# Kernel tuning notes

Hardware: AMD Instinct MI355X
Metric: run time of the kernel (lower is better)

The kernel has to match this reference:

```python
import jax, jax.numpy as jnp
import numpy as np

N_NODES = 100000
N_EDGES = 1600000
D = 128
N_LAYERS = 3
BN_EPS = 1e-5
NORM_EPS = 1e-12


def setup_inputs() -> dict:
    key = jax.random.key(0)
    ks = jax.random.split(key, 4)
    x = jax.random.normal(ks[0], (N_NODES, D), dtype=jnp.float32)
    edge_index = jax.random.randint(ks[1], (2, N_EDGES), 0, N_NODES, dtype=jnp.int32)
    W1 = jax.random.normal(ks[2], (N_LAYERS, D, D), dtype=jnp.float32) * (1.0 / np.sqrt(D))
    W2 = jax.random.normal(ks[3], (N_LAYERS, D, D), dtype=jnp.float32) * (1.0 / np.sqrt(D))
    return {
        "x": x,
        "edge_index": edge_index,
        "W1": W1,
        "b1": jnp.zeros((N_LAYERS, D), jnp.float32),
        "g1": jnp.ones((N_LAYERS, D), jnp.float32),
        "be1": jnp.zeros((N_LAYERS, D), jnp.float32),
        "W2": W2,
        "b2": jnp.zeros((N_LAYERS, D), jnp.float32),
        "g_out": jnp.ones((N_LAYERS - 1, D), jnp.float32),
        "b_out": jnp.zeros((N_LAYERS - 1, D), jnp.float32),
    }


def _batchnorm(h, gamma, beta):
    # BatchNorm1d in training mode: biased batch statistics over nodes.
    mu = jnp.mean(h, axis=0)
    var = jnp.var(h, axis=0)
    return (h - mu) * jax.lax.rsqrt(var + BN_EPS) * gamma + beta


def reference(x, edge_index, W1, b1, g1, be1, W2, b2, g_out, b_out):
    src, dst = edge_index[0], edge_index[1]
    h = x
    for i in range(N_LAYERS):
        # GINConv, eps=0: (1+eps)*x + sum of neighbor messages (scatter-add)
        agg = jax.ops.segment_sum(h[src], dst, num_segments=N_NODES)
        h = h + agg
        # inner MLP: Linear -> BN -> ReLU -> Linear
        h = h @ W1[i] + b1[i]
        h = jax.nn.relu(_batchnorm(h, g1[i], be1[i]))
        h = h @ W2[i] + b2[i]
        if i < N_LAYERS - 1:
            h = jax.nn.relu(_batchnorm(h, g_out[i], b_out[i]))
    # F.normalize(p=2, dim=-1) clamps the norm at 1e-12
    norm = jnp.linalg.norm(h, axis=-1, keepdims=True)
    return h / jnp.maximum(norm, NORM_EPS)
```

## Files before the change

### kernel.cpp

```cpp
#include <hip/hip_runtime.h>

#define M_NODES 100000
#define PADM 100032
#define DIM 128
#define N_EDGES_TOT 1600000
#define NBKT 256
#define NPB 391
#define BKT_CAP 8192
#define INVN 1e-5f
#define NREP 8

typedef unsigned int uint;
typedef unsigned short ushort;
typedef __attribute__((ext_vector_type(8))) short bf16x8;
typedef __attribute__((ext_vector_type(4))) float f32x4;

__device__ __forceinline__ float bflo(uint u) { return __uint_as_float(u << 16); }
__device__ __forceinline__ float bfhi(uint u) { return __uint_as_float(u & 0xffff0000u); }
__device__ __forceinline__ float bf2f(ushort h) { return __uint_as_float(((uint)h) << 16); }
__device__ __forceinline__ ushort f2bf(float f) {
    uint u = __float_as_uint(f);
    return (ushort)((u + 0x7fffu + ((u >> 16) & 1u)) >> 16);
}

__global__ void k_zerof(float* p, int n) {
    int i = blockIdx.x * 256 + threadIdx.x;
    if (i < n) p[i] = 0.f;
}

__global__ void k_cvt(const float* __restrict__ x, ushort* __restrict__ xb,
                      int n4) {
    int i = blockIdx.x * 256 + threadIdx.x;
    if (i >= n4) return;
    float4 v = ((const float4*)x)[i];
    uint2 r;
    r.x = (uint)f2bf(v.x) | ((uint)f2bf(v.y) << 16);
    r.y = (uint)f2bf(v.z) | ((uint)f2bf(v.w) << 16);
    ((uint2*)xb)[i] = r;
}

__global__ void k_wprep(const float* __restrict__ W1,
                        const float* __restrict__ W2, ushort* __restrict__ Wh,
                        ushort* __restrict__ Wl) {
    int i = blockIdx.x * 256 + threadIdx.x;
    if (i >= 6 * 16384) return;
    int l = i >> 14;
    int r = i & 16383;
    int n = r >> 7, k = r & 127;
    const float* W = (l < 3) ? (W1 + l * 16384) : (W2 + (l - 3) * 16384);
    float w = W[k * 128 + n];
    ushort h = f2bf(w);
    Wh[i] = h;
    Wl[i] = f2bf(w - bf2f(h));
}

__global__ void k_bhist(const int* __restrict__ dst, int* __restrict__ cntM,
                        int nE, int nChunks) {
    __shared__ int h[NBKT];
    const int chunk = blockIdx.x, t = threadIdx.x;
    h[t] = 0;
    __syncthreads();
    const int e0 = chunk * 2048;
#pragma unroll
    for (int k = 0; k < 8; ++k) {
        int e = e0 + k * 256 + t;
        if (e < nE) atomicAdd(&h[dst[e] / NPB], 1);
    }
    __syncthreads();
    cntM[t * nChunks + chunk] = h[t];
}

__global__ void k_scanA(int* __restrict__ cnt, int* __restrict__ bsum, int n) {
    __shared__ int s[256];
    int t = threadIdx.x, i = blockIdx.x * 256 + t;
    int v = (i < n) ? cnt[i] : 0;
    s[t] = v;
    __syncthreads();
#pragma unroll
    for (int o = 1; o < 256; o <<= 1) {
        int a = (t >= o) ? s[t - o] : 0;
        __syncthreads();
        s[t] += a;
        __syncthreads();
    }
    if (i < n) cnt[i] = s[t] - v;
    if (t == 255) bsum[blockIdx.x] = s[255];
}

__global__ void k_scanB(int* bsum, int nB) {
    __shared__ int s[1024];
    int t = threadIdx.x;
    int v = (t < nB) ? bsum[t] : 0;
    s[t] = v;
    __syncthreads();
#pragma unroll
    for (int o = 1; o < 1024; o <<= 1) {
        int a = (t >= o) ? s[t - o] : 0;
        __syncthreads();
        s[t] += a;
        __syncthreads();
    }
    if (t < nB) bsum[t] = s[t] - v;
}

__global__ void k_scanC(int* __restrict__ excl, const int* __restrict__ bsum) {
    int i = blockIdx.x * 256 + threadIdx.x;
    excl[i] += bsum[blockIdx.x];
}

__global__ void k_pairs(const int* __restrict__ src, const int* __restrict__ dst,
                        const int* __restrict__ exclM, int2* __restrict__ pairs,
                        int nE, int nChunks) {
    __shared__ int base[NBKT];
    const int chunk = blockIdx.x, t = threadIdx.x;
    base[t] = exclM[t * nChunks + chunk];
    __syncthreads();
    const int e0 = chunk * 2048;
#pragma unroll
    for (int k = 0; k < 8; ++k) {
        int e = e0 + k * 256 + t;
        if (e < nE) {
            int d = dst[e];
            int pos = atomicAdd(&base[d / NPB], 1);
            pairs[pos] = make_int2(d, src[e]);
        }
    }
}

__global__ void k_csrD(const int2* __restrict__ pairs,
                       const int* __restrict__ exclM, int nChunks,
                       int* __restrict__ rowptr, int* __restrict__ srcs,
                       int nE) {
    __shared__ int cnt[512];
    __shared__ int scn[512];
    __shared__ int sl[BKT_CAP];
    const int b = blockIdx.x, t = threadIdx.x;
    const int base = exclM[b * nChunks];
    const int next = (b == NBKT - 1) ? nE : exclM[(b + 1) * nChunks];
    const int count = next - base;
    const int nodeBase = b * NPB;
    const int nNodes = min(NPB, M_NODES - nodeBase);
    cnt[t] = 0;
    cnt[t + 256] = 0;
    __syncthreads();
    for (int i = t; i < count; i += 256)
        atomicAdd(&cnt[pairs[base + i].x - nodeBase], 1);
    __syncthreads();
    scn[t] = cnt[t];
    scn[t + 256] = cnt[t + 256];
    __syncthreads();
#pragma unroll
    for (int o = 1; o < 512; o <<= 1) {
        int a0 = (t >= o) ? scn[t - o] : 0;
        int a1 = scn[t + 256 - o];
        __syncthreads();
        scn[t] += a0;
        scn[t + 256] += a1;
        __syncthreads();
    }
    int o0 = scn[t] - cnt[t];
    int o1 = scn[t + 256] - cnt[t + 256];
    __syncthreads();
    cnt[t] = o0;
    cnt[t + 256] = o1;
    if (t < nNodes) rowptr[nodeBase + t] = base + o0;
    if (t + 256 < nNodes) rowptr[nodeBase + t + 256] = base + o1;
    if (b == 0 && t == 0) rowptr[M_NODES] = nE;
    __syncthreads();
    const bool inLds = (count <= BKT_CAP);
    for (int i = t; i < count; i += 256) {
        int2 p = pairs[base + i];
        int pos = atomicAdd(&cnt[p.x - nodeBase], 1);
        if (inLds) sl[pos] = p.y;
        else srcs[base + pos] = p.y;
    }
    __syncthreads();
    if (inLds)
        for (int i = t; i < count; i += 256) srcs[base + i] = sl[i];
}

__global__ void k_gather(const ushort* __restrict__ h,
                         const int* __restrict__ rowptr,
                         const int* __restrict__ srcs,
                         const float* __restrict__ bnstats,
                         const float* __restrict__ gamma,
                         const float* __restrict__ beta,
                         ushort* __restrict__ AGh, ushort* __restrict__ AGl,
                         int M) {
    int t = threadIdx.x;
    int node = blockIdx.x * 16 + (t >> 4);
    if (node >= M) return;
    int c = (t & 15) * 8;
    const bool bn = (bnstats != nullptr);
    float sc[8], sh[8];
    if (bn) {
#pragma unroll
        for (int e = 0; e < 8; ++e) { sc[e] = 0.f; sh[e] = 0.f; }
        for (int r = 0; r < NREP; ++r) {
            const float* bp = bnstats + r * 256;
#pragma unroll
            for (int e = 0; e < 8; ++e) {
                sc[e] += bp[c + e];
                sh[e] += bp[128 + c + e];
            }
        }
#pragma unroll
        for (int e = 0; e < 8; ++e) {
            float mu = sc[e] * INVN;
            float var = sh[e] * INVN - mu * mu;
            float s = gamma[c + e] * rsqrtf(var + 1e-5f);
            sc[e] = s;
            sh[e] = beta[c + e] - mu * s;
        }
    }
    int beg = rowptr[node];
    int end = rowptr[node + 1];

    float a[8], b[8];
    {
        uint4 v = *(const uint4*)(h + (size_t)node * DIM + c);
        uint u[4] = {v.x, v.y, v.z, v.w};
#pragma unroll
        for (int e = 0; e < 4; ++e) {
            a[2 * e] = bflo(u[e]);
            a[2 * e + 1] = bfhi(u[e]);
        }
        if (bn) {
#pragma unroll
            for (int e = 0; e < 8; ++e)
                a[e] = fmaxf(fmaf(a[e], sc[e], sh[e]), 0.f);
        }
#pragma unroll
        for (int e = 0; e < 8; ++e) b[e] = 0.f;
    }

    int j = beg;
    for (; j + 4 <= end; j += 4) {
        int s0 = srcs[j], s1 = srcs[j + 1], s2 = srcs[j + 2], s3 = srcs[j + 3];
        uint4 g0 = *(const uint4*)(h + (size_t)s0 * DIM + c);
        uint4 g1 = *(const uint4*)(h + (size_t)s1 * DIM + c);
        uint4 g2 = *(const uint4*)(h + (size_t)s2 * DIM + c);
        uint4 g3 = *(const uint4*)(h + (size_t)s3 * DIM + c);
        uint u0[4] = {g0.x, g0.y, g0.z, g0.w};
        uint u1[4] = {g1.x, g1.y, g1.z, g1.w};
        uint u2[4] = {g2.x, g2.y, g2.z, g2.w};
        uint u3[4] = {g3.x, g3.y, g3.z, g3.w};
        if (bn) {
#pragma unroll
            for (int e = 0; e < 4; ++e) {
                a[2 * e] += fmaxf(fmaf(bflo(u0[e]), sc[2 * e], sh[2 * e]), 0.f);
                a[2 * e + 1] += fmaxf(fmaf(bfhi(u0[e]), sc[2 * e + 1], sh[2 * e + 1]), 0.f);
                b[2 * e] += fmaxf(fmaf(bflo(u1[e]), sc[2 * e], sh[2 * e]), 0.f);
                b[2 * e + 1] += fmaxf(fmaf(bfhi(u1[e]), sc[2 * e + 1], sh[2 * e + 1]), 0.f);
                a[2 * e] += fmaxf(fmaf(bflo(u2[e]), sc[2 * e], sh[2 * e]), 0.f);
                a[2 * e + 1] += fmaxf(fmaf(bfhi(u2[e]), sc[2 * e + 1], sh[2 * e + 1]), 0.f);
                b[2 * e] += fmaxf(fmaf(bflo(u3[e]), sc[2 * e], sh[2 * e]), 0.f);
                b[2 * e + 1] += fmaxf(fmaf(bfhi(u3[e]), sc[2 * e + 1], sh[2 * e + 1]), 0.f);
            }
        } else {
#pragma unroll
            for (int e = 0; e < 4; ++e) {
                a[2 * e] += bflo(u0[e]) + bflo(u2[e]);
                a[2 * e + 1] += bfhi(u0[e]) + bfhi(u2[e]);
                b[2 * e] += bflo(u1[e]) + bflo(u3[e]);
                b[2 * e + 1] += bfhi(u1[e]) + bfhi(u3[e]);
            }
        }
    }
    for (; j < end; ++j) {
        int s = srcs[j];
        uint4 g = *(const uint4*)(h + (size_t)s * DIM + c);
        uint u[4] = {g.x, g.y, g.z, g.w};
        if (bn) {
#pragma unroll
            for (int e = 0; e < 4; ++e) {
                a[2 * e] += fmaxf(fmaf(bflo(u[e]), sc[2 * e], sh[2 * e]), 0.f);
                a[2 * e + 1] += fmaxf(fmaf(bfhi(u[e]), sc[2 * e + 1], sh[2 * e + 1]), 0.f);
            }
        } else {
#pragma unroll
            for (int e = 0; e < 4; ++e) {
                a[2 * e] += bflo(u[e]);
                a[2 * e + 1] += bfhi(u[e]);
            }
        }
    }
    uint ho[4], lo4[4];
#pragma unroll
    for (int e = 0; e < 4; ++e) {
        float v0 = a[2 * e] + b[2 * e];
        float v1 = a[2 * e + 1] + b[2 * e + 1];
        ushort h0 = f2bf(v0), h1 = f2bf(v1);
        ho[e] = (uint)h0 | ((uint)h1 << 16);
        lo4[e] = (uint)f2bf(v0 - bf2f(h0)) | ((uint)f2bf(v1 - bf2f(h1)) << 16);
    }
    size_t ix = (size_t)node * DIM + c;
    *(uint4*)(AGh + ix) = make_uint4(ho[0], ho[1], ho[2], ho[3]);
    *(uint4*)(AGl + ix) = make_uint4(lo4[0], lo4[1], lo4[2], lo4[3]);
}

__global__ void __launch_bounds__(256, 3) k_gemmA(
    ushort* __restrict__ Ah, const ushort* __restrict__ Al,
    const ushort* __restrict__ Wh, const ushort* __restrict__ Wl,
    const float* __restrict__ bias, float* __restrict__ statSlot, int M) {
    __shared__ ushort lds[16384];
    const int t = threadIdx.x;
    const int w = t >> 6, lane = t & 63, rq = lane >> 4, rc = lane & 15;
    const int row0 = blockIdx.x * 64;

    bf16x8 wh[4][2], wl[4][2];
#pragma unroll
    for (int kc = 0; kc < 4; ++kc)
#pragma unroll
        for (int jj = 0; jj < 2; ++jj) {
            size_t off = (size_t)(w * 32 + jj * 16 + rc) * DIM + kc * 32 + rq * 8;
            wh[kc][jj] = *(const bf16x8*)(Wh + off);
            wl[kc][jj] = *(const bf16x8*)(Wl + off);
        }

#pragma unroll
    for (int i = 0; i < 8; ++i) {
        int idx = t + i * 256;
        int pl = idx >> 10;
        int r = (idx >> 4) & 63;
        int cb = idx & 15;
        const ushort* p = pl ? Al : Ah;
        uint4 v = *(const uint4*)(p + (size_t)(row0 + r) * DIM + cb * 8);
        *(uint4*)((char*)lds + pl * 16384 + r * 256 +
                  ((cb * 16) ^ ((r & 15) << 4))) = v;
    }
    __syncthreads();

    f32x4 acc[4][2];
#pragma unroll
    for (int i = 0; i < 4; ++i)
#pragma unroll
        for (int jj = 0; jj < 2; ++jj) acc[i][jj] = (f32x4){0.f, 0.f, 0.f, 0.f};

#pragma unroll
    for (int kc = 0; kc < 4; ++kc) {
        const int kb = kc * 64 + rq * 16;
#pragma unroll
        for (int i = 0; i < 4; ++i) {
            int lr = i * 16 + rc;
            int so = lr * 256 + (kb ^ ((lr & 15) << 4));
            bf16x8 ah = *(const bf16x8*)((char*)lds + so);
            bf16x8 al = *(const bf16x8*)((char*)lds + 16384 + so);
#pragma unroll
            for (int jj = 0; jj < 2; ++jj) {
                acc[i][jj] = __builtin_amdgcn_mfma_f32_16x16x32_bf16(ah, wh[kc][jj], acc[i][jj], 0, 0, 0);
                acc[i][jj] = __builtin_amdgcn_mfma_f32_16x16x32_bf16(al, wh[kc][jj], acc[i][jj], 0, 0, 0);
                acc[i][jj] = __builtin_amdgcn_mfma_f32_16x16x32_bf16(ah, wl[kc][jj], acc[i][jj], 0, 0, 0);
            }
        }
    }

    float bc[2] = {bias[w * 32 + rc], bias[w * 32 + 16 + rc]};
    float csum[2] = {0.f, 0.f}, csq[2] = {0.f, 0.f};

    __syncthreads();
#pragma unroll
    for (int i = 0; i < 4; ++i)
#pragma unroll
        for (int r = 0; r < 4; ++r) {
            int lrow = i * 16 + rq * 4 + r;
            bool live = (row0 + lrow) < M;
#pragma unroll
            for (int jj = 0; jj < 2; ++jj) {
                float o = acc[i][jj][r] + bc[jj];
                int off = lrow * 256 +
                          (((w * 32 + jj * 16 + rc) * 2) ^ ((lrow & 15) << 4));
                *(ushort*)((char*)lds + off) = f2bf(o);
                if (live) { csum[jj] += o; csq[jj] += o * o; }
            }
        }
    __syncthreads();
    {
        int lrow = w * 16 + (lane & 15);
        int kq = lane >> 4;
        ushort* dH = Ah + (size_t)row0 * DIM;
#pragma unroll
        for (int kc = 0; kc < 4; ++kc) {
            int off = lrow * 256 + ((kc * 64 + kq * 16) ^ ((lrow & 15) << 4));
            uint4 H = *(uint4*)((char*)lds + off);
            size_t go = ((size_t)(w * 4 + kc) * 64 + lane) * 8;
            *(uint4*)(dH + go) = H;
        }
    }
#pragma unroll
    for (int jj = 0; jj < 2; ++jj) {
        csum[jj] += __shfl_xor(csum[jj], 16);
        csum[jj] += __shfl_xor(csum[jj], 32);
        csq[jj] += __shfl_xor(csq[jj], 16);
        csq[jj] += __shfl_xor(csq[jj], 32);
    }
    float* slot = statSlot + (blockIdx.x & (NREP - 1)) * 256;
    if (lane < 16) {
        atomicAdd(slot + w * 32 + rc, csum[0]);
        atomicAdd(slot + w * 32 + 16 + rc, csum[1]);
        atomicAdd(slot + 128 + w * 32 + rc, csq[0]);
        atomicAdd(slot + 128 + w * 32 + 16 + rc, csq[1]);
    }
}

__global__ void __launch_bounds__(256, 4) k_gemmB(
    const ushort* __restrict__ Ch,
    const ushort* __restrict__ Wh, const ushort* __restrict__ Wl,
    const float* __restrict__ bias, const float* __restrict__ bnstats,
    const float* __restrict__ gamma, const float* __restrict__ beta,
    ushort* __restrict__ Cb, float* __restrict__ outF,
    float* __restrict__ statSlot, int M) {
    __shared__ char smem[16384];
    const int t = threadIdx.x;
    const int w = t >> 6, lane = t & 63, rq = lane >> 4, rc = lane & 15;
    const int row0 = blockIdx.x * 64;

    bf16x8 wh[4][2], wl[4][2];
#pragma unroll
    for (int kc = 0; kc < 4; ++kc)
#pragma unroll
        for (int jj = 0; jj < 2; ++jj) {
            size_t off = (size_t)(w * 32 + jj * 16 + rc) * DIM + kc * 32 + rq * 8;
            wh[kc][jj] = *(const bf16x8*)(Wh + off);
            wl[kc][jj] = *(const bf16x8*)(Wl + off);
        }

    float* coef = (float*)smem;
    if (t < 128) {
        float s0 = 0.f, q0 = 0.f;
#pragma unroll
        for (int r = 0; r < NREP; ++r) {
            s0 += bnstats[r * 256 + t];
            q0 += bnstats[r * 256 + 128 + t];
        }
        float mu = s0 * INVN;
        float var = q0 * INVN - mu * mu;
        float s = gamma[t] * rsqrtf(var + 1e-5f);
        coef[t] = s;
        coef[128 + t] = beta[t] - mu * s;
    }
    __syncthreads();

    const ushort* pH = Ch + (size_t)row0 * DIM;
    const int kq8 = (lane >> 4) * 8;

    f32x4 acc[4][2];
#pragma unroll
    for (int i = 0; i < 4; ++i)
#pragma unroll
        for (int jj = 0; jj < 2; ++jj) acc[i][jj] = (f32x4){0.f, 0.f, 0.f, 0.f};

#pragma unroll
    for (int kc = 0; kc < 4; ++kc) {
        float sc8[8], sh8[8];
#pragma unroll
        for (int e = 0; e < 8; ++e) {
            sc8[e] = coef[kc * 32 + kq8 + e];
            sh8[e] = coef[128 + kc * 32 + kq8 + e];
        }
#pragma unroll
        for (int i = 0; i < 4; ++i) {
            size_t go = ((size_t)(i * 4 + kc) * 64 + lane) * 8;
            uint4 H = *(const uint4*)(pH + go);
            uint hu[4] = {H.x, H.y, H.z, H.w};
            uint oh[4], ol[4];
#pragma unroll
            for (int e = 0; e < 4; ++e) {
                float v0 = bflo(hu[e]);
                float v1 = bfhi(hu[e]);
                v0 = fmaxf(fmaf(v0, sc8[2 * e], sh8[2 * e]), 0.f);
                v1 = fmaxf(fmaf(v1, sc8[2 * e + 1], sh8[2 * e + 1]), 0.f);
                ushort h0 = f2bf(v0), h1 = f2bf(v1);
                oh[e] = (uint)h0 | ((uint)h1 << 16);
                ol[e] = (uint)f2bf(v0 - bf2f(h0)) |
                        ((uint)f2bf(v1 - bf2f(h1)) << 16);
            }
            uint4 AH = make_uint4(oh[0], oh[1], oh[2], oh[3]);
            uint4 AL = make_uint4(ol[0], ol[1], ol[2], ol[3]);
            bf16x8 ah = *(bf16x8*)&AH;
            bf16x8 al = *(bf16x8*)&AL;
#pragma unroll
            for (int jj = 0; jj < 2; ++jj) {
                acc[i][jj] = __builtin_amdgcn_mfma_f32_16x16x32_bf16(ah, wh[kc][jj], acc[i][jj], 0, 0, 0);
                acc[i][jj] = __builtin_amdgcn_mfma_f32_16x16x32_bf16(al, wh[kc][jj], acc[i][jj], 0, 0, 0);
                acc[i][jj] = __builtin_amdgcn_mfma_f32_16x16x32_bf16(ah, wl[kc][jj], acc[i][jj], 0, 0, 0);
            }
        }
    }

    float bc[2] = {bias[w * 32 + rc], bias[w * 32 + 16 + rc]};

    if (outF) {
#pragma unroll
        for (int i = 0; i < 4; ++i)
#pragma unroll
            for (int r = 0; r < 4; ++r)
#pragma unroll
                for (int jj = 0; jj < 2; ++jj) acc[i][jj][r] += bc[jj];
        __syncthreads();
        float* nr = (float*)smem;
#pragma unroll
        for (int i = 0; i < 4; ++i)
#pragma unroll
            for (int r = 0; r < 4; ++r) {
                float ss = acc[i][0][r] * acc[i][0][r] + acc[i][1][r] * acc[i][1][r];
                ss += __shfl_xor(ss, 1);
                ss += __shfl_xor(ss, 2);
                ss += __shfl_xor(ss, 4);
                ss += __shfl_xor(ss, 8);
                if (rc == 0) nr[(i * 16 + rq * 4 + r) * 4 + w] = ss;
            }
        __syncthreads();
#pragma unroll
        for (int i = 0; i < 4; ++i)
#pragma unroll
            for (int r = 0; r < 4; ++r) {
                int lrow = i * 16 + rq * 4 + r;
                float4 q = *(const float4*)(nr + lrow * 4);
                float inv = 1.f / fmaxf(sqrtf(q.x + q.y + q.z + q.w), 1e-12f);
                int row = row0 + lrow;
                if (row < M) {
                    outF[(size_t)row * DIM + w * 32 + rc] = acc[i][0][r] * inv;
                    outF[(size_t)row * DIM + w * 32 + 16 + rc] = acc[i][1][r] * inv;
                }
            }
        return;
    }

    float csum[2] = {0.f, 0.f}, csq[2] = {0.f, 0.f};
    __syncthreads();
#pragma unroll
    for (int i = 0; i < 4; ++i)
#pragma unroll
        for (int r = 0; r < 4; ++r) {
            int lrow = i * 16 + rq * 4 + r;
            bool live = (row0 + lrow) < M;
#pragma unroll
            for (int jj = 0; jj < 2; ++jj) {
                float o = acc[i][jj][r] + bc[jj];
                int off = lrow * 256 +
                          (((w * 32 + jj * 16 + rc) * 2) ^ ((lrow & 15) << 4));
                *(ushort*)(smem + off) = f2bf(o);
                if (live) { csum[jj] += o; csq[jj] += o * o; }
            }
        }
    __syncthreads();
#pragma unroll
    for (int it = 0; it < 4; ++it) {
        int idx = t + it * 256;
        int row = idx >> 4, cb = idx & 15;
        int grow = row0 + row;
        if (grow < M) {
            uint4 v = *(uint4*)(smem + row * 256 + ((cb * 16) ^ ((row & 15) << 4)));
            *(uint4*)(Cb + (size_t)grow * DIM + cb * 8) = v;
        }
    }
#pragma unroll
    for (int jj = 0; jj < 2; ++jj) {
        csum[jj] += __shfl_xor(csum[jj], 16);
        csum[jj] += __shfl_xor(csum[jj], 32);
        csq[jj] += __shfl_xor(csq[jj], 16);
        csq[jj] += __shfl_xor(csq[jj], 32);
    }
    float* slot = statSlot + (blockIdx.x & (NREP - 1)) * 256;
    if (lane < 16) {
        atomicAdd(slot + w * 32 + rc, csum[0]);
        atomicAdd(slot + w * 32 + 16 + rc, csum[1]);
        atomicAdd(slot + 128 + w * 32 + rc, csq[0]);
        atomicAdd(slot + 128 + w * 32 + 16 + rc, csq[1]);
    }
}

extern "C" void kernel_launch(void* const* d_in, const int* in_sizes, int n_in,
                              void* d_out, int out_size, void* d_ws,
                              size_t ws_size, hipStream_t stream) {
    const float* x = (const float*)d_in[0];
    const int* ei = (const int*)d_in[1];
    const float* W1 = (const float*)d_in[2];
    const float* b1 = (const float*)d_in[3];
    const float* g1 = (const float*)d_in[4];
    const float* be1 = (const float*)d_in[5];
    const float* W2 = (const float*)d_in[6];
    const float* b2 = (const float*)d_in[7];
    const float* g_out = (const float*)d_in[8];
    const float* b_out = (const float*)d_in[9];
    float* out = (float*)d_out;

    const int M = M_NODES;
    const int E = N_EDGES_TOT;
    const size_t NM = (size_t)M * DIM;
    const size_t PM = (size_t)PADM * DIM;
    const int nChunks = (E + 2047) / 2048;
    const int nMat = NBKT * nChunks;
    const int SLOT = 256 * NREP;

    ushort* AGh = (ushort*)d_ws;
    ushort* AGl = AGh + PM;
    ushort* B0 = AGl + PM;
    ushort* Wh = B0 + NM;
    ushort* Wl = Wh + 6 * 16384;
    float* st = (float*)(Wl + 6 * 16384);
    float* stA0 = st;
    float* stA1 = st + SLOT;
    float* stA2 = st + 2 * SLOT;
    float* stB0 = st + 3 * SLOT;
    float* stB1 = st + 4 * SLOT;
    int2* pairs = (int2*)(st + 5 * SLOT);
    int* rowptr = (int*)(pairs + E);
    int* cntM = rowptr + (M + 2);
    int* bsum = cntM + nMat;
    int* srcs = bsum + 1024;

    const int* src = ei;
    const int* dst = ei + E;

    const int gemmGrid = PADM / 64;
    const int gathGrid = (M + 15) / 16;

    k_bhist<<<nChunks, 256, 0, stream>>>(dst, cntM, E, nChunks);
    k_scanA<<<nMat / 256, 256, 0, stream>>>(cntM, bsum, nMat);
    k_scanB<<<1, 1024, 0, stream>>>(bsum, nMat / 256);
    k_scanC<<<nMat / 256, 256, 0, stream>>>(cntM, bsum);
    k_pairs<<<nChunks, 256, 0, stream>>>(src, dst, cntM, pairs, E, nChunks);
    k_csrD<<<NBKT, 256, 0, stream>>>(pairs, cntM, nChunks, rowptr, srcs, E);

    k_cvt<<<(int)((NM / 4 + 255) / 256), 256, 0, stream>>>(x, B0, (int)(NM / 4));
    k_wprep<<<(6 * 16384 + 255) / 256, 256, 0, stream>>>(W1, W2, Wh, Wl);
    k_zerof<<<(5 * SLOT + 255) / 256, 256, 0, stream>>>(st, 5 * SLOT);

    k_gather<<<gathGrid, 256, 0, stream>>>(B0, rowptr, srcs, nullptr, nullptr,
                                           nullptr, AGh, AGl, M);
    k_gemmA<<<gemmGrid, 256, 0, stream>>>(AGh, AGl, Wh, Wl, b1, stA0, M);
    k_gemmB<<<gemmGrid, 256, 0, stream>>>(AGh, Wh + 3 * 16384, Wl + 3 * 16384,
                                          b2, stA0, g1, be1, B0, nullptr, stB0, M);

    k_gather<<<gathGrid, 256, 0, stream>>>(B0, rowptr, srcs, stB0, g_out, b_out,
                                           AGh, AGl, M);
    k_gemmA<<<gemmGrid, 256, 0, stream>>>(AGh, AGl, Wh + 16384, Wl + 16384,
                                          b1 + 128, stA1, M);
    k_gemmB<<<gemmGrid, 256, 0, stream>>>(AGh, Wh + 4 * 16384, Wl + 4 * 16384,
                                          b2 + 128, stA1, g1 + 128, be1 + 128,
                                          B0, nullptr, stB1, M);

    k_gather<<<gathGrid, 256, 0, stream>>>(B0, rowptr, srcs, stB1, g_out + 128,
                                           b_out + 128, AGh, AGl, M);
    k_gemmA<<<gemmGrid, 256, 0, stream>>>(AGh, AGl, Wh + 2 * 16384, Wl + 2 * 16384,
                                          b1 + 256, stA2, M);
    k_gemmB<<<gemmGrid, 256, 0, stream>>>(AGh, Wh + 5 * 16384, Wl + 5 * 16384,
                                          b2 + 256, stA2, g1 + 256, be1 + 256,
                                          nullptr, out, nullptr, M);
}
```

Measured before the change: 487.1 us.

## Apply output BatchNorm-ReLU in a separate in-place pass, simplify gather to 4 channels/thread

Moves the inter-layer BatchNorm+ReLU out of the neighbor gather into a new elementwise kernel that rewrites the bf16 activations in place once per node. The gather then sums raw rows, and each thread handles 4 channels with 8-byte loads and 32 threads per node instead of 16. This removes the per-edge FMA/max work and the per-thread reduction of the statistics replicas, at the cost of an extra full read/write pass over the activations. It also adds a second bf16 rounding after normalization.

```diff
diff --git a/kernel.cpp b/kernel.cpp
--- a/kernel.cpp
+++ b/kernel.cpp
@@ -52,6 +52,41 @@
     ushort h = f2bf(w);
     Wh[i] = h;
     Wl[i] = f2bf(w - bf2f(h));
+}
+
+__global__ void k_bnr(ushort* __restrict__ B0,
+                      const float* __restrict__ bnstats,
+                      const float* __restrict__ gamma,
+                      const float* __restrict__ beta, int n4) {
+    __shared__ float coef[256];
+    int t = threadIdx.x;
+    if (t < 128) {
+        float s0 = 0.f, q0 = 0.f;
+#pragma unroll
+        for (int r = 0; r < NREP; ++r) {
+            s0 += bnstats[r * 256 + t];
+            q0 += bnstats[r * 256 + 128 + t];
+        }
+        float mu = s0 * INVN;
+        float var = q0 * INVN - mu * mu;
+        float s = gamma[t] * rsqrtf(var + 1e-5f);
+        coef[t] = s;
+        coef[128 + t] = beta[t] - mu * s;
+    }
+    __syncthreads();
+    for (int i = blockIdx.x * 256 + t; i < n4; i += gridDim.x * 256) {
+        uint4 v = ((const uint4*)B0)[i];
+        int c0 = (i & 15) * 8;
+        uint u[4] = {v.x, v.y, v.z, v.w};
+        uint o[4];
+#pragma unroll
+        for (int e = 0; e < 4; ++e) {
+            float v0 = fmaxf(fmaf(bflo(u[e]), coef[c0 + 2 * e], coef[128 + c0 + 2 * e]), 0.f);
+            float v1 = fmaxf(fmaf(bfhi(u[e]), coef[c0 + 2 * e + 1], coef[128 + c0 + 2 * e + 1]), 0.f);
+            o[e] = (uint)f2bf(v0) | ((uint)f2bf(v1) << 16);
+        }
+        ((uint4*)B0)[i] = make_uint4(o[0], o[1], o[2], o[3]);
+    }
 }
 
 __global__ void k_bhist(const int* __restrict__ dst, int* __restrict__ cntM,
@@ -182,121 +217,48 @@
 __global__ void k_gather(const ushort* __restrict__ h,
                          const int* __restrict__ rowptr,
                          const int* __restrict__ srcs,
-                         const float* __restrict__ bnstats,
-                         const float* __restrict__ gamma,
-                         const float* __restrict__ beta,
                          ushort* __restrict__ AGh, ushort* __restrict__ AGl,
                          int M) {
     int t = threadIdx.x;
-    int node = blockIdx.x * 16 + (t >> 4);
+    int node = blockIdx.x * 8 + (t >> 5);
     if (node >= M) return;
-    int c = (t & 15) * 8;
-    const bool bn = (bnstats != nullptr);
-    float sc[8], sh[8];
-    if (bn) {
-#pragma unroll
-        for (int e = 0; e < 8; ++e) { sc[e] = 0.f; sh[e] = 0.f; }
-        for (int r = 0; r < NREP; ++r) {
-            const float* bp = bnstats + r * 256;
-#pragma unroll
-            for (int e = 0; e < 8; ++e) {
-                sc[e] += bp[c + e];
-                sh[e] += bp[128 + c + e];
-            }
-        }
-#pragma unroll
-        for (int e = 0; e < 8; ++e) {
-            float mu = sc[e] * INVN;
-            float var = sh[e] * INVN - mu * mu;
-            float s = gamma[c + e] * rsqrtf(var + 1e-5f);
-            sc[e] = s;
-            sh[e] = beta[c + e] - mu * s;
-        }
-    }
+    int c = (t & 31) * 4;
     int beg = rowptr[node];
     int end = rowptr[node + 1];
 
-    float a[8], b[8];
-    {
-        uint4 v = *(const uint4*)(h + (size_t)node * DIM + c);
-        uint u[4] = {v.x, v.y, v.z, v.w};
-#pragma unroll
-        for (int e = 0; e < 4; ++e) {
-            a[2 * e] = bflo(u[e]);
-            a[2 * e + 1] = bfhi(u[e]);
-        }
-        if (bn) {
-#pragma unroll
-            for (int e = 0; e < 8; ++e)
-                a[e] = fmaxf(fmaf(a[e], sc[e], sh[e]), 0.f);
-        }
-#pragma unroll
-        for (int e = 0; e < 8; ++e) b[e] = 0.f;
-    }
+    uint2 v = *(const uint2*)(h + (size_t)node * DIM + c);
+    float a0 = bflo(v.x), a1 = bfhi(v.x), a2 = bflo(v.y), a3 = bfhi(v.y);
+    float b0 = 0.f, b1 = 0.f, b2 = 0.f, b3 = 0.f;
 
     int j = beg;
     for (; j + 4 <= end; j += 4) {
         int s0 = srcs[j], s1 = srcs[j + 1], s2 = srcs[j + 2], s3 = srcs[j + 3];
-        uint4 g0 = *(const uint4*)(h + (size_t)s0 * DIM + c);
-        uint4 g1 = *(const uint4*)(h + (size_t)s1 * DIM + c);
-        uint4 g2 = *(const uint4*)(h + (size_t)s2 * DIM + c);
-        uint4 g3 = *(const uint4*)(h + (size_t)s3 * DIM + c);
-        uint u0[4] = {g0.x, g0.y, g0.z, g0.w};
-        uint u1[4] = {g1.x, g1.y, g1.z, g1.w};
-        uint u2[4] = {g2.x, g2.y, g2.z, g2.w};
-        uint u3[4] = {g3.x, g3.y, g3.z, g3.w};
-        if (bn) {
-#pragma unroll
-            for (int e = 0; e < 4; ++e) {
-                a[2 * e] += fmaxf(fmaf(bflo(u0[e]), sc[2 * e], sh[2 * e]), 0.f);
-                a[2 * e + 1] += fmaxf(fmaf(bfhi(u0[e]), sc[2 * e + 1], sh[2 * e + 1]), 0.f);
-                b[2 * e] += fmaxf(fmaf(bflo(u1[e]), sc[2 * e], sh[2 * e]), 0.f);
-                b[2 * e + 1] += fmaxf(fmaf(bfhi(u1[e]), sc[2 * e + 1], sh[2 * e + 1]), 0.f);
-                a[2 * e] += fmaxf(fmaf(bflo(u2[e]), sc[2 * e], sh[2 * e]), 0.f);
-                a[2 * e + 1] += fmaxf(fmaf(bfhi(u2[e]), sc[2 * e + 1], sh[2 * e + 1]), 0.f);
-                b[2 * e] += fmaxf(fmaf(bflo(u3[e]), sc[2 * e], sh[2 * e]), 0.f);
-                b[2 * e + 1] += fmaxf(fmaf(bfhi(u3[e]), sc[2 * e + 1], sh[2 * e + 1]), 0.f);
-            }
-        } else {
-#pragma unroll
-            for (int e = 0; e < 4; ++e) {
-                a[2 * e] += bflo(u0[e]) + bflo(u2[e]);
-                a[2 * e + 1] += bfhi(u0[e]) + bfhi(u2[e]);
-                b[2 * e] += bflo(u1[e]) + bflo(u3[e]);
-                b[2 * e + 1] += bfhi(u1[e]) + bfhi(u3[e]);
-            }
-        }
+        uint2 g0 = *(const uint2*)(h + (size_t)s0 * DIM + c);
+        uint2 g1 = *(const uint2*)(h + (size_t)s1 * DIM + c);
+        uint2 g2 = *(const uint2*)(h + (size_t)s2 * DIM + c);
+        uint2 g3 = *(const uint2*)(h + (size_t)s3 * DIM + c);
+        a0 += bflo(g0.x); a1 += bfhi(g0.x); a2 += bflo(g0.y); a3 += bfhi(g0.y);
+        b0 += bflo(g1.x); b1 += bfhi(g1.x); b2 += bflo(g1.y); b3 += bfhi(g1.y);
+        a0 += bflo(g2.x); a1 += bfhi(g2.x); a2 += bflo(g2.y); a3 += bfhi(g2.y);
+        b0 += bflo(g3.x); b1 += bfhi(g3.x); b2 += bflo(g3.y); b3 += bfhi(g3.y);
     }
     for (; j < end; ++j) {
         int s = srcs[j];
-        uint4 g = *(const uint4*)(h + (size_t)s * DIM + c);
-        uint u[4] = {g.x, g.y, g.z, g.w};
-        if (bn) {
-#pragma unroll
-            for (int e = 0; e < 4; ++e) {
-                a[2 * e] += fmaxf(fmaf(bflo(u[e]), sc[2 * e], sh[2 * e]), 0.f);
-                a[2 * e + 1] += fmaxf(fmaf(bfhi(u[e]), sc[2 * e + 1], sh[2 * e + 1]), 0.f);
-            }
-        } else {
-#pragma unroll
-            for (int e = 0; e < 4; ++e) {
-                a[2 * e] += bflo(u[e]);
-                a[2 * e + 1] += bfhi(u[e]);
-            }
-        }
-    }
-    uint ho[4], lo4[4];
-#pragma unroll
-    for (int e = 0; e < 4; ++e) {
-        float v0 = a[2 * e] + b[2 * e];
-        float v1 = a[2 * e + 1] + b[2 * e + 1];
-        ushort h0 = f2bf(v0), h1 = f2bf(v1);
-        ho[e] = (uint)h0 | ((uint)h1 << 16);
-        lo4[e] = (uint)f2bf(v0 - bf2f(h0)) | ((uint)f2bf(v1 - bf2f(h1)) << 16);
-    }
+        uint2 g = *(const uint2*)(h + (size_t)s * DIM + c);
+        a0 += bflo(g.x); a1 += bfhi(g.x); a2 += bflo(g.y); a3 += bfhi(g.y);
+    }
+    float s0 = a0 + b0, s1 = a1 + b1, s2 = a2 + b2, s3 = a3 + b3;
+    ushort h0 = f2bf(s0), h1 = f2bf(s1), h2 = f2bf(s2), h3 = f2bf(s3);
+    ushort l0 = f2bf(s0 - bf2f(h0)), l1 = f2bf(s1 - bf2f(h1));
+    ushort l2 = f2bf(s2 - bf2f(h2)), l3 = f2bf(s3 - bf2f(h3));
+    uint2 hp, lp;
+    hp.x = (uint)h0 | ((uint)h1 << 16);
+    hp.y = (uint)h2 | ((uint)h3 << 16);
+    lp.x = (uint)l0 | ((uint)l1 << 16);
+    lp.y = (uint)l2 | ((uint)l3 << 16);
     size_t ix = (size_t)node * DIM + c;
-    *(uint4*)(AGh + ix) = make_uint4(ho[0], ho[1], ho[2], ho[3]);
-    *(uint4*)(AGl + ix) = make_uint4(lo4[0], lo4[1], lo4[2], lo4[3]);
+    *(uint2*)(AGh + ix) = hp;
+    *(uint2*)(AGl + ix) = lp;
 }
 
 __global__ void __launch_bounds__(256, 3) k_gemmA(
@@ -615,7 +577,8 @@
     const int* dst = ei + E;
 
     const int gemmGrid = PADM / 64;
-    const int gathGrid = (M + 15) / 16;
+    const int gathGrid = (M + 7) / 8;
+    const int n4 = (int)(NM / 8);
 
     k_bhist<<<nChunks, 256, 0, stream>>>(dst, cntM, E, nChunks);
     k_scanA<<<nMat / 256, 256, 0, stream>>>(cntM, bsum, nMat);
@@ -628,22 +591,21 @@
     k_wprep<<<(6 * 16384 + 255) / 256, 256, 0, stream>>>(W1, W2, Wh, Wl);
     k_zerof<<<(5 * SLOT + 255) / 256, 256, 0, stream>>>(st, 5 * SLOT);
 
-    k_gather<<<gathGrid, 256, 0, stream>>>(B0, rowptr, srcs, nullptr, nullptr,
-                                           nullptr, AGh, AGl, M);
+    k_gather<<<gathGrid, 256, 0, stream>>>(B0, rowptr, srcs, AGh, AGl, M);
     k_gemmA<<<gemmGrid, 256, 0, stream>>>(AGh, AGl, Wh, Wl, b1, stA0, M);
     k_gemmB<<<gemmGrid, 256, 0, stream>>>(AGh, Wh + 3 * 16384, Wl + 3 * 16384,
                                           b2, stA0, g1, be1, B0, nullptr, stB0, M);
-
-    k_gather<<<gathGrid, 256, 0, stream>>>(B0, rowptr, srcs, stB0, g_out, b_out,
-                                           AGh, AGl, M);
+    k_bnr<<<2048, 256, 0, stream>>>(B0, stB0, g_out, b_out, n4);
+
+    k_gather<<<gathGrid, 256, 0, stream>>>(B0, rowptr, srcs, AGh, AGl, M);
     k_gemmA<<<gemmGrid, 256, 0, stream>>>(AGh, AGl, Wh + 16384, Wl + 16384,
                                           b1 + 128, stA1, M);
     k_gemmB<<<gemmGrid, 256, 0, stream>>>(AGh, Wh + 4 * 16384, Wl + 4 * 16384,
                                           b2 + 128, stA1, g1 + 128, be1 + 128,
                                           B0, nullptr, stB1, M);
-
-    k_gather<<<gathGrid, 256, 0, stream>>>(B0, rowptr, srcs, stB1, g_out + 128,
-                                           b_out + 128, AGh, AGl, M);
+    k_bnr<<<2048, 256, 0, stream>>>(B0, stB1, g_out + 128, b_out + 128, n4);
+
+    k_gather<<<gathGrid, 256, 0, stream>>>(B0, rowptr, srcs, AGh, AGl, M);
     k_gemmA<<<gemmGrid, 256, 0, stream>>>(AGh, AGl, Wh + 2 * 16384, Wl + 2 * 16384,
                                           b1 + 256, stA2, M);
     k_gemmB<<<gemmGrid, 256, 0, stream>>>(AGh, Wh + 5 * 16384, Wl + 5 * 16384,
```

New measurement: 467.8 us. 3.9% less time.
